# Performance work log

Hardware: AMD Instinct MI355X
Metric: run time of the kernel (lower is better)

Reference implementation:

```python
import jax, jax.numpy as jnp
import numpy as np
import math

# AF2 IPA dims
B, N = 1, 768
C1, C2 = 384, 128          # single / pair channels
H = 12                     # heads
SQK, SV = 16, 16           # scalar qk / v per head
PQK, PV = 4, 8             # point qk / v per head


def quat_to_rot(quat):
    # quat [..., 4] -> rotation matrix [..., 3, 3] (normalized, as QuatAffine.from_tensor)
    q = quat / jnp.linalg.norm(quat, axis=-1, keepdims=True)
    w, x, y, z = q[..., 0], q[..., 1], q[..., 2], q[..., 3]
    r0 = jnp.stack([1 - 2 * (y * y + z * z), 2 * (x * y - w * z), 2 * (x * z + w * y)], axis=-1)
    r1 = jnp.stack([2 * (x * y + w * z), 1 - 2 * (x * x + z * z), 2 * (y * z - w * x)], axis=-1)
    r2 = jnp.stack([2 * (x * z - w * y), 2 * (y * z + w * x), 1 - 2 * (x * x + y * y)], axis=-1)
    return jnp.stack([r0, r1, r2], axis=-2)


def setup_inputs():
    key = jax.random.key(0)
    ks = jax.random.split(key, 10)

    def lin(k, fan_in, fan_out):
        lim = 1.0 / np.sqrt(fan_in)
        kw, kb = jax.random.split(k)
        W = jax.random.uniform(kw, (fan_in, fan_out), minval=-lim, maxval=lim, dtype=jnp.float32)
        b = jax.random.uniform(kb, (fan_out,), minval=-lim, maxval=lim, dtype=jnp.float32)
        return W, b

    q_w, q_b = lin(ks[0], C1, SQK * H)
    kv_w, kv_b = lin(ks[1], C1, (SQK + SV) * H)
    qp_w, qp_b = lin(ks[2], C1, PQK * H * 3)
    kvp_w, kvp_b = lin(ks[3], C1, (PQK + PV) * H * 3)
    w2d_w, w2d_b = lin(ks[4], C2, H)
    fin_w, fin_b = lin(ks[5], H * (C2 + SV + 4 * PV), C1)

    rec_1d = jax.random.normal(ks[6], (B, N, C1), dtype=jnp.float32)
    rep_2d = jax.random.normal(ks[7], (B, N, N, C2), dtype=jnp.float32)
    rec_T = jax.random.normal(ks[8], (B, N, 7), dtype=jnp.float32)
    trainable_w = jnp.zeros((H,), dtype=jnp.float32)

    return dict(rec_1d=rec_1d, rep_2d=rep_2d, rec_T=rec_T,
                q_w=q_w, q_b=q_b, kv_w=kv_w, kv_b=kv_b,
                qp_w=qp_w, qp_b=qp_b, kvp_w=kvp_w, kvp_b=kvp_b,
                w2d_w=w2d_w, w2d_b=w2d_b, fin_w=fin_w, fin_b=fin_b,
                trainable_w=trainable_w)


def ipa_forward(rec_1d, rep_2d, rec_T, q_w, q_b, kv_w, kv_b, qp_w, qp_b,
                kvp_w, kvp_b, w2d_w, w2d_b, fin_w, fin_b, trainable_w):
    R = quat_to_rot(rec_T[..., :4])          # [B,N,3,3]
    t = rec_T[..., 4:]                       # [B,N,3]

    # scalar q/k/v: [B,N,H,S]
    q_scalar = (rec_1d @ q_w + q_b).reshape(B, N, H, SQK)
    kv_scalar = (rec_1d @ kv_w + kv_b).reshape(B, N, H, SQK + SV)
    k_scalar, v_scalar = kv_scalar[..., :SQK], kv_scalar[..., SQK:]

    # point q: split last dim into thirds (x,y,z blocks), rotate to global frame
    qp = (rec_1d @ qp_w + qp_b).reshape(B, N, 3, H * PQK)
    qp_glob = jnp.einsum('bnic,bncd->bnid', R, qp) + t[..., None]
    q_pt = jnp.transpose(qp_glob.reshape(B, N, 3, H, PQK), (0, 3, 1, 4, 2))  # [B,H,N,PQK,3]

    kvp = (rec_1d @ kvp_w + kvp_b).reshape(B, N, 3, H * (PQK + PV))
    kvp_glob = jnp.einsum('bnic,bncd->bnid', R, kvp) + t[..., None]
    kvp_pt = jnp.transpose(kvp_glob.reshape(B, N, 3, H, PQK + PV), (0, 3, 1, 4, 2))  # [B,H,N,P,3]
    k_pt, v_pt = kvp_pt[..., :PQK, :], kvp_pt[..., PQK:, :]

    # logit weights
    num_logit_terms = 3
    scalar_weights = math.sqrt(1.0 / (num_logit_terms * SQK))
    point_weights = math.sqrt(1.0 / (num_logit_terms * PQK * 9.0 / 2))
    pw = point_weights * jax.nn.softplus(trainable_w)  # [H]

    # point-distance logits: [B,H,Nq,Nk]
    dist = jnp.sum(jnp.square(q_pt[:, :, :, None, :, :] - k_pt[:, :, None, :, :, :]), axis=-1)
    attn_qk_point = -0.5 * jnp.einsum('h,bhqkp->bhqk', pw, dist)

    # scalar logits
    attn_qk_scalar = jnp.einsum('bqhs,bkhs->bhqk', scalar_weights * q_scalar, k_scalar)

    # pair bias
    attn_2d = (rep_2d @ w2d_w + w2d_b)                       # [B,N,N,H]
    attn_2d = math.sqrt(1.0 / num_logit_terms) * jnp.transpose(attn_2d, (0, 3, 1, 2))

    attn = jax.nn.softmax(attn_qk_scalar + attn_qk_point + attn_2d, axis=-1)  # [B,H,Nq,Nk]

    # scalar output
    result_scalar = jnp.einsum('bhqk,bkhs->bqhs', attn, v_scalar).reshape(B, N, H * SV)

    # point output -> back to local frame
    res_pt = jnp.einsum('bhqk,bhkpc->bhqpc', attn, v_pt)                 # [B,H,N,PV,3]
    g = jnp.transpose(res_pt, (0, 2, 4, 1, 3)).reshape(B, N, 3, H * PV)  # [B,N,3,H*PV]
    local = jnp.einsum('bnci,bncd->bnid', R, g - t[..., None])           # R^T (g - t)
    pt_norm = jnp.sqrt(1e-8 + jnp.sum(jnp.square(local), axis=2))        # [B,N,H*PV]

    # pair output
    att2d = jnp.einsum('bhij,bijc->bihc', attn, rep_2d).reshape(B, N, H * C2)

    final_act = jnp.concatenate(
        [result_scalar, local[:, :, 0], local[:, :, 1], local[:, :, 2], pt_norm, att2d], axis=-1)
    return final_act @ fin_w + fin_b  # [B,N,C1]


def reference(rec_1d, rep_2d, rec_T, q_w, q_b, kv_w, kv_b, qp_w, qp_b,
              kvp_w, kvp_b, w2d_w, w2d_b, fin_w, fin_b, trainable_w):
    return ipa_forward(rec_1d, rep_2d, rec_T, q_w, q_b, kv_w, kv_b, qp_w, qp_b,
                       kvp_w, kvp_b, w2d_w, w2d_b, fin_w, fin_b, trainable_w)
```

## Files before the change

kernel.cpp:

```cpp
#include <hip/hip_runtime.h>
#include <math.h>


namespace {
constexpr int NRES = 768;
constexpr int C1V  = 384;

constexpr size_t OFF_R     = 0;
constexpr size_t OFF_T     = 10240;
constexpr size_t OFF_PW    = 13824;
constexpr size_t OFF_W2DT  = 13952;
constexpr size_t OFF_WPACK = 16384;
constexpr size_t OFF_BPACK = 458752;
constexpr size_t OFF_PROJ  = 460800;
constexpr size_t OFF_QPT   = 1345536;
constexpr size_t OFF_KPT   = 1456128;
constexpr size_t OFF_VPTT  = 1566720;
constexpr size_t OFF_VST   = 1787904;
constexpr size_t OFF_FA    = 1935360;
constexpr size_t OFF_PART  = 3557376;
}

__global__ void k0_prep(const float* __restrict__ recT,
                        const float* __restrict__ tw,
                        const float* __restrict__ w2d,
                        float* __restrict__ ws) {
  int gid = blockIdx.x * 256 + threadIdx.x;
  if (gid < NRES) {
    float w = recT[gid*7+0], x = recT[gid*7+1], y = recT[gid*7+2], z = recT[gid*7+3];
    float inv = rsqrtf(w*w + x*x + y*y + z*z);
    w *= inv; x *= inv; y *= inv; z *= inv;
    float* r = ws + OFF_R + (size_t)gid*12;
    r[0] = 1.f-2.f*(y*y+z*z); r[1] = 2.f*(x*y-w*z);     r[2] = 2.f*(x*z+w*y);
    r[3] = 2.f*(x*y+w*z);     r[4] = 1.f-2.f*(x*x+z*z); r[5] = 2.f*(y*z-w*x);
    r[6] = 2.f*(x*z-w*y);     r[7] = 2.f*(y*z+w*x);     r[8] = 1.f-2.f*(x*x+y*y);
    float* tv = ws + OFF_T + (size_t)gid*4;
    tv[0] = recT[gid*7+4]; tv[1] = recT[gid*7+5]; tv[2] = recT[gid*7+6]; tv[3] = 0.f;
  } else if (gid < NRES + 12) {
    int h = gid - NRES;
    (ws + OFF_PW)[h] = sqrtf(1.f/54.f) * log1pf(expf(tw[h]));
  } else if (gid < NRES + 12 + 1536) {
    int idx = gid - NRES - 12;
    int h = idx % 12, c = idx / 12;
    (ws + OFF_W2DT)[h*128 + c] = w2d[c*12 + h];
  }
}

__global__ void k0b_pack(const float* __restrict__ qw,  const float* __restrict__ qb,
                         const float* __restrict__ kvw, const float* __restrict__ kvb,
                         const float* __restrict__ qpw, const float* __restrict__ qpb,
                         const float* __restrict__ kvpw,const float* __restrict__ kvpb,
                         float* __restrict__ ws) {
  int idx = blockIdx.x * 256 + threadIdx.x;
  if (idx < 384*1152) {
    int k = idx / 1152, col = idx % 1152;
    float v;
    if (col < 192)      v = qw[(size_t)k*192 + col];
    else if (col < 576) v = kvw[(size_t)k*384 + (col-192)];
    else if (col < 720) v = qpw[(size_t)k*144 + (col-576)];
    else                v = kvpw[(size_t)k*432 + (col-720)];
    (ws + OFF_WPACK)[idx] = v;
  } else if (idx < 384*1152 + 1152) {
    int col = idx - 384*1152;
    float v;
    if (col < 192)      v = qb[col];
    else if (col < 576) v = kvb[col-192];
    else if (col < 720) v = qpb[col-576];
    else                v = kvpb[col-720];
    (ws + OFF_BPACK)[col] = v;
  }
}

__global__ __launch_bounds__(256) void k1_proj(const float* __restrict__ x,
                                               float* __restrict__ ws) {
  int bi = blockIdx.x, bo = blockIdx.y, t = threadIdx.x;
  __shared__ float AsT[16*68];
  __shared__ float Bs[16*68];
  const float* W = ws + OFF_WPACK;
  float accv[4][4] = {};
  int i0 = bi*64, o0 = bo*64;
  int ti = t >> 4, to = t & 15;
  for (int kt = 0; kt < 24; kt++) {
    int k0 = kt*16;
    {
      int r = t >> 2, kq = t & 3;
      float4 a = *(const float4*)(x + (size_t)(i0+r)*C1V + k0 + kq*4);
      AsT[(kq*4+0)*68 + r] = a.x;
      AsT[(kq*4+1)*68 + r] = a.y;
      AsT[(kq*4+2)*68 + r] = a.z;
      AsT[(kq*4+3)*68 + r] = a.w;
      int kr = t >> 4, ol = t & 15;
      *(float4*)&Bs[kr*68 + ol*4] =
          *(const float4*)(W + (size_t)(k0+kr)*1152 + o0 + ol*4);
    }
    __syncthreads();
    for (int k = 0; k < 16; k++) {
      float4 a4 = *(float4*)&AsT[k*68 + ti*4];
      float4 b4 = *(float4*)&Bs[k*68 + to*4];
      accv[0][0] += a4.x*b4.x; accv[0][1] += a4.x*b4.y; accv[0][2] += a4.x*b4.z; accv[0][3] += a4.x*b4.w;
      accv[1][0] += a4.y*b4.x; accv[1][1] += a4.y*b4.y; accv[1][2] += a4.y*b4.z; accv[1][3] += a4.y*b4.w;
      accv[2][0] += a4.z*b4.x; accv[2][1] += a4.z*b4.y; accv[2][2] += a4.z*b4.z; accv[2][3] += a4.z*b4.w;
      accv[3][0] += a4.w*b4.x; accv[3][1] += a4.w*b4.y; accv[3][2] += a4.w*b4.z; accv[3][3] += a4.w*b4.w;
    }
    __syncthreads();
  }
  float* proj = ws + OFF_PROJ;
  const float* bp = ws + OFF_BPACK;
  #pragma unroll
  for (int ii = 0; ii < 4; ii++) {
    int orow = i0 + ti*4 + ii;
    int ocol = o0 + to*4;
    float4 bv = *(const float4*)(bp + ocol);
    float4 v = make_float4(accv[ii][0]+bv.x, accv[ii][1]+bv.y,
                           accv[ii][2]+bv.z, accv[ii][3]+bv.w);
    *(float4*)&proj[(size_t)orow*1152 + ocol] = v;
  }
}

__global__ __launch_bounds__(256) void k2_frames(float* __restrict__ ws) {
  int i = blockIdx.x, t = threadIdx.x;
  const float* R  = ws + OFF_R + (size_t)i*12;
  const float* tv = ws + OFF_T + (size_t)i*4;
  const float* prow = ws + OFF_PROJ + (size_t)i*1152;
  if (t < 144) {
    int d = t % 48, ci = t / 48;
    const float* qp = prow + 576;
    float v = R[ci*3+0]*qp[0*48+d] + R[ci*3+1]*qp[1*48+d] + R[ci*3+2]*qp[2*48+d] + tv[ci];
    int h = d / 4, p = d % 4;
    (ws + OFF_QPT)[(size_t)i*144 + h*12 + p*3 + ci] = v;
  }
  for (int r = 0; r < 2; r++) {
    int item = t + r*256;
    if (item < 432) {
      int d = item % 144, ci = item / 144;
      const float* kp = prow + 720;
      float v = R[ci*3+0]*kp[0*144+d] + R[ci*3+1]*kp[1*144+d] + R[ci*3+2]*kp[2*144+d] + tv[ci];
      int h = d / 12, pp = d % 12;
      if (pp < 4)
        (ws + OFF_KPT)[(size_t)i*144 + h*12 + pp*3 + ci] = v;
      else
        (ws + OFF_VPTT)[((size_t)(h*8 + (pp-4))*3 + ci)*768 + i] = v;
    }
  }
  if (t < 192) {
    int h = t / 16, s = t % 16;
    (ws + OFF_VST)[(size_t)t*768 + i] = prow[192 + h*32 + 16 + s];
  }
}

__global__ __launch_bounds__(256) void k_att(const float* __restrict__ rep,
                                             const float* __restrict__ w2db_,
                                             float* __restrict__ ws) {
  __shared__ float tile[64*132];
  __shared__ float ptile[12*64];
  __shared__ float wds[12*128];
  __shared__ float qsl[192], qptl[144];
  __shared__ float mrow[12], srow[12], frow[12], tmaxs[12], w2dbl[12], pwl[12];

  int i = blockIdx.x, t = threadIdx.x;
  int w = __builtin_amdgcn_readfirstlane(t >> 6);
  int lane = t & 63;

  for (int u = t; u < 1536; u += 256) wds[u] = (ws + OFF_W2DT)[u];
  if (t < 192) qsl[t]  = (ws + OFF_PROJ)[(size_t)i*1152 + t];
  if (t < 144) qptl[t] = (ws + OFF_QPT)[(size_t)i*144 + t];
  if (t < 12) {
    mrow[t] = -1e30f; srow[t] = 0.f;
    pwl[t] = (ws + OFF_PW)[t];
    w2dbl[t] = w2db_[t];
  }
  float acc2d[12][2];
  #pragma unroll
  for (int h = 0; h < 12; h++) { acc2d[h][0] = 0.f; acc2d[h][1] = 0.f; }
  int h0, h1 = -1;
  const float* vrow0; const float* vrow1 = nullptr;
  if (t < 192) { h0 = t >> 4; vrow0 = ws + OFF_VST + (size_t)t*768; }
  else { int u = t - 192; h0 = u/24; vrow0 = ws + OFF_VPTT + (size_t)u*768; }
  if (t < 224) { int u = t + 64; h1 = u/24; vrow1 = ws + OFF_VPTT + (size_t)u*768; }
  float accV0 = 0.f, accV1 = 0.f;
  __syncthreads();

  const float sw  = 0.14433756729740643f;
  const float c2d = 0.5773502691896258f;

  for (int tt = 0; tt < 12; tt++) {
    int j0 = tt*64;
    #pragma unroll
    for (int k = 0; k < 8; k++) {
      int u = t + k*256;
      int row = u >> 5, c4 = u & 31;
      *(float4*)&tile[row*132 + c4*4] =
          *(const float4*)&rep[((size_t)i*768 + (j0+row))*128 + c4*4];
    }
    __syncthreads();

    float a2d[3] = {0.f, 0.f, 0.f};
    for (int c4 = 0; c4 < 32; c4++) {
      float4 v = *(float4*)&tile[lane*132 + c4*4];
      #pragma unroll
      for (int hh = 0; hh < 3; hh++) {
        float4 wv = *(float4*)&wds[(w*3+hh)*128 + c4*4];
        a2d[hh] += v.x*wv.x + v.y*wv.y + v.z*wv.z + v.w*wv.w;
      }
    }
    int j = j0 + lane;
    const float* ksr  = ws + OFF_PROJ + (size_t)j*1152 + 192;
    const float* kptr = ws + OFF_KPT + (size_t)j*144;
    float l[3], tm[3];
    #pragma unroll
    for (int hh = 0; hh < 3; hh++) {
      int h = w*3 + hh;
      float ds_ = 0.f;
      #pragma unroll
      for (int s4 = 0; s4 < 4; s4++) {
        float4 q4 = *(const float4*)(qsl + h*16 + s4*4);
        float4 k4 = *(const float4*)(ksr + h*32 + s4*4);
        ds_ += q4.x*k4.x + q4.y*k4.y + q4.z*k4.z + q4.w*k4.w;
      }
      float dp = 0.f;
      #pragma unroll
      for (int pc = 0; pc < 3; pc++) {
        float4 q4 = *(const float4*)(qptl + h*12 + pc*4);
        float4 k4 = *(const float4*)(kptr + h*12 + pc*4);
        float dx = q4.x-k4.x, dy = q4.y-k4.y, dz = q4.z-k4.z, dw = q4.w-k4.w;
        dp += dx*dx + dy*dy + dz*dz + dw*dw;
      }
      l[hh] = sw*ds_ - 0.5f*pwl[h]*dp + c2d*(a2d[hh] + w2dbl[h]);
      float m = l[hh];
      #pragma unroll
      for (int d = 1; d < 64; d <<= 1) m = fmaxf(m, __shfl_xor(m, d));
      tm[hh] = m;
    }
    if (lane == 0) {
      tmaxs[w*3+0] = tm[0]; tmaxs[w*3+1] = tm[1]; tmaxs[w*3+2] = tm[2];
    }
    __syncthreads();

    if (t < 12) {
      float mo = mrow[t];
      float mn = fmaxf(mo, tmaxs[t]);
      frow[t] = __expf(mo - mn);
      mrow[t] = mn;
    }
    __syncthreads();

    #pragma unroll
    for (int hh = 0; hh < 3; hh++) {
      int h = w*3 + hh;
      float p = __expf(l[hh] - mrow[h]);
      ptile[h*64 + lane] = p;
      float s = p;
      #pragma unroll
      for (int d = 1; d < 64; d <<= 1) s += __shfl_xor(s, d);
      if (lane == 0) srow[h] = srow[h]*frow[h] + s;
    }
    __syncthreads();

    #pragma unroll
    for (int h = 0; h < 12; h++) {
      float fh = frow[h];
      acc2d[h][0] *= fh; acc2d[h][1] *= fh;
    }
    int jb = w*16;
    for (int jj = 0; jj < 16; jj++) {
      int jl = jb + jj;
      float2 r2 = *(float2*)&tile[jl*132 + lane*2];
      #pragma unroll
      for (int h = 0; h < 12; h++) {
        float p = ptile[h*64 + jl];
        acc2d[h][0] += p*r2.x; acc2d[h][1] += p*r2.y;
      }
    }
    {
      float a = accV0 * frow[h0];
      const float* vr = vrow0 + j0;
      for (int q = 0; q < 16; q++) {
        float4 v4 = *(const float4*)(vr + q*4);
        a += ptile[h0*64+q*4+0]*v4.x + ptile[h0*64+q*4+1]*v4.y
           + ptile[h0*64+q*4+2]*v4.z + ptile[h0*64+q*4+3]*v4.w;
      }
      accV0 = a;
    }
    if (h1 >= 0) {
      float a = accV1 * frow[h1];
      const float* vr = vrow1 + j0;
      for (int q = 0; q < 16; q++) {
        float4 v4 = *(const float4*)(vr + q*4);
        a += ptile[h1*64+q*4+0]*v4.x + ptile[h1*64+q*4+1]*v4.y
           + ptile[h1*64+q*4+2]*v4.z + ptile[h1*64+q*4+3]*v4.w;
      }
      accV1 = a;
    }
    __syncthreads();
  }

  float* fa = ws + OFF_FA + (size_t)i*2112;
  float* respt = ptile;
  if (t < 192) fa[t] = accV0 / srow[h0];
  else respt[t - 192] = accV0 / srow[h0];
  if (h1 >= 0) respt[t + 64] = accV1 / srow[h1];
  float* redbuf = tile;
  #pragma unroll
  for (int h = 0; h < 12; h++) {
    redbuf[w*1536 + h*128 + lane*2 + 0] = acc2d[h][0];
    redbuf[w*1536 + h*128 + lane*2 + 1] = acc2d[h][1];
  }
  __syncthreads();
  for (int r = 0; r < 6; r++) {
    int u = t + r*256;
    int h = u >> 7;
    float v = redbuf[u] + redbuf[1536+u] + redbuf[3072+u] + redbuf[4608+u];
    fa[576 + u] = v / srow[h];
  }
  if (t < 96) {
    const float* R  = ws + OFF_R + (size_t)i*12;
    const float* tv = ws + OFF_T + (size_t)i*4;
    float g0 = respt[t*3+0] - tv[0];
    float g1 = respt[t*3+1] - tv[1];
    float g2 = respt[t*3+2] - tv[2];
    float l0 = R[0]*g0 + R[3]*g1 + R[6]*g2;
    float l1 = R[1]*g0 + R[4]*g1 + R[7]*g2;
    float l2 = R[2]*g0 + R[5]*g1 + R[8]*g2;
    fa[192 + 0*96 + t] = l0;
    fa[192 + 1*96 + t] = l1;
    fa[192 + 2*96 + t] = l2;
    fa[480 + t] = sqrtf(1e-8f + l0*l0 + l1*l1 + l2*l2);
  }
}

__global__ __launch_bounds__(256) void k7_gemm(const float* __restrict__ finw,
                                               float* __restrict__ ws) {
  int bi = blockIdx.x, bo = blockIdx.y, bz = blockIdx.z, t = threadIdx.x;
  __shared__ float AsT[16*68];
  __shared__ float Bs[16*68];
  const float* fa = ws + OFF_FA;
  float accv[4][4] = {};
  int i0 = bi*64, o0 = bo*64;
  int ti = t >> 4, to = t & 15;
  for (int kt = 0; kt < 33; kt++) {
    int k0 = bz*528 + kt*16;
    {
      int r = t >> 2, kq = t & 3;
      float4 a = *(const float4*)(fa + (size_t)(i0+r)*2112 + k0 + kq*4);
      AsT[(kq*4+0)*68 + r] = a.x;
      AsT[(kq*4+1)*68 + r] = a.y;
      AsT[(kq*4+2)*68 + r] = a.z;
      AsT[(kq*4+3)*68 + r] = a.w;
      int kr = t >> 4, ol = t & 15;
      *(float4*)&Bs[kr*68 + ol*4] =
          *(const float4*)(finw + (size_t)(k0+kr)*384 + o0 + ol*4);
    }
    __syncthreads();
    for (int k = 0; k < 16; k++) {
      float4 a4 = *(float4*)&AsT[k*68 + ti*4];
      float4 b4 = *(float4*)&Bs[k*68 + to*4];
      accv[0][0] += a4.x*b4.x; accv[0][1] += a4.x*b4.y; accv[0][2] += a4.x*b4.z; accv[0][3] += a4.x*b4.w;
      accv[1][0] += a4.y*b4.x; accv[1][1] += a4.y*b4.y; accv[1][2] += a4.y*b4.z; accv[1][3] += a4.y*b4.w;
      accv[2][0] += a4.z*b4.x; accv[2][1] += a4.z*b4.y; accv[2][2] += a4.z*b4.z; accv[2][3] += a4.z*b4.w;
      accv[3][0] += a4.w*b4.x; accv[3][1] += a4.w*b4.y; accv[3][2] += a4.w*b4.z; accv[3][3] += a4.w*b4.w;
    }
    __syncthreads();
  }
  float* part = ws + OFF_PART + (size_t)bz*768*384;
  #pragma unroll
  for (int ii = 0; ii < 4; ii++) {
    float4 v = make_float4(accv[ii][0], accv[ii][1], accv[ii][2], accv[ii][3]);
    *(float4*)&part[(size_t)(i0 + ti*4 + ii)*384 + o0 + to*4] = v;
  }
}

__global__ void k8_out(const float* __restrict__ finb,
                       const float* __restrict__ ws,
                       float* __restrict__ out) {
  int idx = blockIdx.x*256 + threadIdx.x;
  int o = idx % 384;
  const float* part = ws + OFF_PART;
  out[idx] = part[idx] + part[294912 + idx] + part[2*294912 + idx]
           + part[3*294912 + idx] + finb[o];
}

extern "C" void kernel_launch(void* const* d_in, const int* in_sizes, int n_in,
                              void* d_out, int out_size, void* d_ws, size_t ws_size,
                              hipStream_t stream) {
  const float* rec1d = (const float*)d_in[0];
  const float* rep2d = (const float*)d_in[1];
  const float* recT  = (const float*)d_in[2];
  const float* qw    = (const float*)d_in[3];
  const float* qb    = (const float*)d_in[4];
  const float* kvw   = (const float*)d_in[5];
  const float* kvb   = (const float*)d_in[6];
  const float* qpw   = (const float*)d_in[7];
  const float* qpb   = (const float*)d_in[8];
  const float* kvpw  = (const float*)d_in[9];
  const float* kvpb  = (const float*)d_in[10];
  const float* w2dw  = (const float*)d_in[11];
  const float* w2db  = (const float*)d_in[12];
  const float* finw  = (const float*)d_in[13];
  const float* finb  = (const float*)d_in[14];
  const float* tw    = (const float*)d_in[15];
  float* ws  = (float*)d_ws;
  float* out = (float*)d_out;

  hipLaunchKernelGGL(k0_prep, dim3(10), dim3(256), 0, stream, recT, tw, w2dw, ws);
  hipLaunchKernelGGL(k0b_pack, dim3(1733), dim3(256), 0, stream,
                     qw, qb, kvw, kvb, qpw, qpb, kvpw, kvpb, ws);
  hipLaunchKernelGGL(k1_proj, dim3(12, 18), dim3(256), 0, stream, rec1d, ws);
  hipLaunchKernelGGL(k2_frames, dim3(768), dim3(256), 0, stream, ws);
  hipLaunchKernelGGL(k_att, dim3(768), dim3(256), 0, stream, rep2d, w2db, ws);
  hipLaunchKernelGGL(k7_gemm, dim3(12, 6, 4), dim3(256), 0, stream, finw, ws);
  hipLaunchKernelGGL(k8_out, dim3(1152), dim3(256), 0, stream, finb, ws, out);
}
```

Baseline: 0.9998 ms.

## Split attention over key chunks with wave-local softmax and a combine kernel

Measured after the change: 2.980 ms. +198.1%, slower.

```diff
diff --git a/kernel.cpp b/kernel.cpp
--- a/kernel.cpp
+++ b/kernel.cpp
@@ -18,6 +18,7 @@
 constexpr size_t OFF_VPTT  = 1566720;
 constexpr size_t OFF_VST   = 1787904;
 constexpr size_t OFF_FA    = 1935360;
+constexpr size_t OFF_PARTIAL = 3557376;
 constexpr size_t OFF_PART  = 3557376;
 }
 
@@ -148,43 +149,52 @@
   }
 }
 
-__global__ __launch_bounds__(256) void k_att(const float* __restrict__ rep,
-                                             const float* __restrict__ w2db_,
-                                             float* __restrict__ ws) {
+__global__ __launch_bounds__(256, 3) void k_att2(const float* __restrict__ rep,
+                                                 const float* __restrict__ w2db_,
+                                                 float* __restrict__ ws) {
   __shared__ float tile[64*132];
-  __shared__ float ptile[12*64];
+  __shared__ float ptile[12*68];
   __shared__ float wds[12*128];
   __shared__ float qsl[192], qptl[144];
-  __shared__ float mrow[12], srow[12], frow[12], tmaxs[12], w2dbl[12], pwl[12];
-
-  int i = blockIdx.x, t = threadIdx.x;
-  int w = __builtin_amdgcn_readfirstlane(t >> 6);
-  int lane = t & 63;
+
+  int jc = blockIdx.x, i = blockIdx.y, t = threadIdx.x;
+  int w = t >> 6, lane = t & 63;
+  int hb = w*3;
 
   for (int u = t; u < 1536; u += 256) wds[u] = (ws + OFF_W2DT)[u];
   if (t < 192) qsl[t]  = (ws + OFF_PROJ)[(size_t)i*1152 + t];
   if (t < 144) qptl[t] = (ws + OFF_QPT)[(size_t)i*144 + t];
-  if (t < 12) {
-    mrow[t] = -1e30f; srow[t] = 0.f;
-    pwl[t] = (ws + OFF_PW)[t];
-    w2dbl[t] = w2db_[t];
-  }
-  float acc2d[12][2];
+  float pwv[3], w2dbv[3];
   #pragma unroll
-  for (int h = 0; h < 12; h++) { acc2d[h][0] = 0.f; acc2d[h][1] = 0.f; }
-  int h0, h1 = -1;
-  const float* vrow0; const float* vrow1 = nullptr;
-  if (t < 192) { h0 = t >> 4; vrow0 = ws + OFF_VST + (size_t)t*768; }
-  else { int u = t - 192; h0 = u/24; vrow0 = ws + OFF_VPTT + (size_t)u*768; }
-  if (t < 224) { int u = t + 64; h1 = u/24; vrow1 = ws + OFF_VPTT + (size_t)u*768; }
+  for (int hh = 0; hh < 3; hh++) {
+    pwv[hh]   = (ws + OFF_PW)[hb+hh];
+    w2dbv[hh] = w2db_[hb+hh];
+  }
+  float m0 = -1e30f, m1 = -1e30f, m2 = -1e30f;
+  float s0 = 0.f, s1 = 0.f, s2 = 0.f;
+  float a2d0[2] = {0.f,0.f}, a2d1[2] = {0.f,0.f}, a2d2[2] = {0.f,0.f};
+
+  int hh0 = (lane < 40) ? 0 : 1;
+  int idx0 = lane - hh0*40;
+  const float* vrow0 = (idx0 < 16)
+      ? ws + OFF_VST  + (size_t)((hb+hh0)*16 + idx0)*768
+      : ws + OFF_VPTT + (size_t)((hb+hh0)*24 + idx0-16)*768;
+  int pr0 = (hb+hh0)*68;
+  int s1i = lane + 64;
+  bool has1 = s1i < 120;
+  int hh1 = (s1i < 80) ? 1 : 2;
+  int idx1 = s1i - hh1*40;
+  const float* vrow1 = (idx1 < 16)
+      ? ws + OFF_VST  + (size_t)((hb+hh1)*16 + idx1)*768
+      : ws + OFF_VPTT + (size_t)((hb+hh1)*24 + idx1-16)*768;
+  int pr1 = (hb+hh1)*68;
   float accV0 = 0.f, accV1 = 0.f;
-  __syncthreads();
 
   const float sw  = 0.14433756729740643f;
   const float c2d = 0.5773502691896258f;
 
-  for (int tt = 0; tt < 12; tt++) {
-    int j0 = tt*64;
+  for (int tt = 0; tt < 3; tt++) {
+    int j0 = jc*192 + tt*64;
     #pragma unroll
     for (int k = 0; k < 8; k++) {
       int u = t + k*256;
@@ -199,17 +209,17 @@
       float4 v = *(float4*)&tile[lane*132 + c4*4];
       #pragma unroll
       for (int hh = 0; hh < 3; hh++) {
-        float4 wv = *(float4*)&wds[(w*3+hh)*128 + c4*4];
+        float4 wv = *(float4*)&wds[(hb+hh)*128 + c4*4];
         a2d[hh] += v.x*wv.x + v.y*wv.y + v.z*wv.z + v.w*wv.w;
       }
     }
     int j = j0 + lane;
     const float* ksr  = ws + OFF_PROJ + (size_t)j*1152 + 192;
     const float* kptr = ws + OFF_KPT + (size_t)j*144;
-    float l[3], tm[3];
+    float l[3];
     #pragma unroll
     for (int hh = 0; hh < 3; hh++) {
-      int h = w*3 + hh;
+      int h = hb + hh;
       float ds_ = 0.f;
       #pragma unroll
       for (int s4 = 0; s4 < 4; s4++) {
@@ -225,93 +235,147 @@
         float dx = q4.x-k4.x, dy = q4.y-k4.y, dz = q4.z-k4.z, dw = q4.w-k4.w;
         dp += dx*dx + dy*dy + dz*dz + dw*dw;
       }
-      l[hh] = sw*ds_ - 0.5f*pwl[h]*dp + c2d*(a2d[hh] + w2dbl[h]);
-      float m = l[hh];
-      #pragma unroll
-      for (int d = 1; d < 64; d <<= 1) m = fmaxf(m, __shfl_xor(m, d));
-      tm[hh] = m;
-    }
-    if (lane == 0) {
-      tmaxs[w*3+0] = tm[0]; tmaxs[w*3+1] = tm[1]; tmaxs[w*3+2] = tm[2];
-    }
-    __syncthreads();
-
-    if (t < 12) {
-      float mo = mrow[t];
-      float mn = fmaxf(mo, tmaxs[t]);
-      frow[t] = __expf(mo - mn);
-      mrow[t] = mn;
-    }
-    __syncthreads();
-
-    #pragma unroll
-    for (int hh = 0; hh < 3; hh++) {
-      int h = w*3 + hh;
-      float p = __expf(l[hh] - mrow[h]);
-      ptile[h*64 + lane] = p;
-      float s = p;
-      #pragma unroll
-      for (int d = 1; d < 64; d <<= 1) s += __shfl_xor(s, d);
-      if (lane == 0) srow[h] = srow[h]*frow[h] + s;
-    }
-    __syncthreads();
-
-    #pragma unroll
-    for (int h = 0; h < 12; h++) {
-      float fh = frow[h];
-      acc2d[h][0] *= fh; acc2d[h][1] *= fh;
-    }
-    int jb = w*16;
-    for (int jj = 0; jj < 16; jj++) {
-      int jl = jb + jj;
-      float2 r2 = *(float2*)&tile[jl*132 + lane*2];
-      #pragma unroll
-      for (int h = 0; h < 12; h++) {
-        float p = ptile[h*64 + jl];
-        acc2d[h][0] += p*r2.x; acc2d[h][1] += p*r2.y;
-      }
-    }
-    {
-      float a = accV0 * frow[h0];
+      l[hh] = sw*ds_ - 0.5f*pwv[hh]*dp + c2d*(a2d[hh] + w2dbv[hh]);
+    }
+
+    float f0, f1, f2;
+    {
+      float mt = l[0];
+      #pragma unroll
+      for (int d = 1; d < 64; d <<= 1) mt = fmaxf(mt, __shfl_xor(mt, d));
+      float mn = fmaxf(m0, mt); f0 = __expf(m0 - mn); m0 = mn;
+      float p = __expf(l[0] - mn); ptile[(hb+0)*68 + lane] = p;
+      float ss = p;
+      #pragma unroll
+      for (int d = 1; d < 64; d <<= 1) ss += __shfl_xor(ss, d);
+      s0 = s0*f0 + ss;
+    }
+    {
+      float mt = l[1];
+      #pragma unroll
+      for (int d = 1; d < 64; d <<= 1) mt = fmaxf(mt, __shfl_xor(mt, d));
+      float mn = fmaxf(m1, mt); f1 = __expf(m1 - mn); m1 = mn;
+      float p = __expf(l[1] - mn); ptile[(hb+1)*68 + lane] = p;
+      float ss = p;
+      #pragma unroll
+      for (int d = 1; d < 64; d <<= 1) ss += __shfl_xor(ss, d);
+      s1 = s1*f1 + ss;
+    }
+    {
+      float mt = l[2];
+      #pragma unroll
+      for (int d = 1; d < 64; d <<= 1) mt = fmaxf(mt, __shfl_xor(mt, d));
+      float mn = fmaxf(m2, mt); f2 = __expf(m2 - mn); m2 = mn;
+      float p = __expf(l[2] - mn); ptile[(hb+2)*68 + lane] = p;
+      float ss = p;
+      #pragma unroll
+      for (int d = 1; d < 64; d <<= 1) ss += __shfl_xor(ss, d);
+      s2 = s2*f2 + ss;
+    }
+
+    a2d0[0] *= f0; a2d0[1] *= f0;
+    a2d1[0] *= f1; a2d1[1] *= f1;
+    a2d2[0] *= f2; a2d2[1] *= f2;
+    for (int jq = 0; jq < 16; jq++) {
+      float4 p0 = *(float4*)&ptile[(hb+0)*68 + jq*4];
+      float4 p1 = *(float4*)&ptile[(hb+1)*68 + jq*4];
+      float4 p2 = *(float4*)&ptile[(hb+2)*68 + jq*4];
+      #pragma unroll
+      for (int r = 0; r < 4; r++) {
+        float2 r2 = *(float2*)&tile[(jq*4+r)*132 + lane*2];
+        float pa = (r==0)?p0.x:(r==1)?p0.y:(r==2)?p0.z:p0.w;
+        float pb = (r==0)?p1.x:(r==1)?p1.y:(r==2)?p1.z:p1.w;
+        float pc = (r==0)?p2.x:(r==1)?p2.y:(r==2)?p2.z:p2.w;
+        a2d0[0] += pa*r2.x; a2d0[1] += pa*r2.y;
+        a2d1[0] += pb*r2.x; a2d1[1] += pb*r2.y;
+        a2d2[0] += pc*r2.x; a2d2[1] += pc*r2.y;
+      }
+    }
+
+    {
+      float fsel = (lane < 40) ? f0 : f1;
+      float a = accV0 * fsel;
       const float* vr = vrow0 + j0;
       for (int q = 0; q < 16; q++) {
         float4 v4 = *(const float4*)(vr + q*4);
-        a += ptile[h0*64+q*4+0]*v4.x + ptile[h0*64+q*4+1]*v4.y
-           + ptile[h0*64+q*4+2]*v4.z + ptile[h0*64+q*4+3]*v4.w;
+        float4 p4 = *(float4*)&ptile[pr0 + q*4];
+        a += p4.x*v4.x + p4.y*v4.y + p4.z*v4.z + p4.w*v4.w;
       }
       accV0 = a;
     }
-    if (h1 >= 0) {
-      float a = accV1 * frow[h1];
+    if (has1) {
+      float fsel = (s1i < 80) ? f1 : f2;
+      float a = accV1 * fsel;
       const float* vr = vrow1 + j0;
       for (int q = 0; q < 16; q++) {
         float4 v4 = *(const float4*)(vr + q*4);
-        a += ptile[h1*64+q*4+0]*v4.x + ptile[h1*64+q*4+1]*v4.y
-           + ptile[h1*64+q*4+2]*v4.z + ptile[h1*64+q*4+3]*v4.w;
+        float4 p4 = *(float4*)&ptile[pr1 + q*4];
+        a += p4.x*v4.x + p4.y*v4.y + p4.z*v4.z + p4.w*v4.w;
       }
       accV1 = a;
     }
     __syncthreads();
   }
 
+  float* part = ws + OFF_PARTIAL + ((size_t)i*4 + jc)*2048;
+  if (lane == 0) {
+    part[hb+0] = m0; part[hb+1] = m1; part[hb+2] = m2;
+    part[12+hb+0] = s0; part[12+hb+1] = s1; part[12+hb+2] = s2;
+  }
+  part[24 + (hb+0)*128 + lane*2 + 0] = a2d0[0];
+  part[24 + (hb+0)*128 + lane*2 + 1] = a2d0[1];
+  part[24 + (hb+1)*128 + lane*2 + 0] = a2d1[0];
+  part[24 + (hb+1)*128 + lane*2 + 1] = a2d1[1];
+  part[24 + (hb+2)*128 + lane*2 + 0] = a2d2[0];
+  part[24 + (hb+2)*128 + lane*2 + 1] = a2d2[1];
+  {
+    int dst0 = (idx0 < 16) ? 1560 + (hb+hh0)*16 + idx0
+                           : 1752 + (hb+hh0)*24 + (idx0-16);
+    part[dst0] = accV0;
+  }
+  if (has1) {
+    int dst1 = (idx1 < 16) ? 1560 + (hb+hh1)*16 + idx1
+                           : 1752 + (hb+hh1)*24 + (idx1-16);
+    part[dst1] = accV1;
+  }
+}
+
+__global__ __launch_bounds__(256) void k_comb(float* __restrict__ ws) {
+  int i = blockIdx.x, t = threadIdx.x;
+  __shared__ float coef[4][12];
+  __shared__ float respt[288];
+  const float* P = ws + OFF_PARTIAL + (size_t)i*4*2048;
+  if (t < 12) {
+    float ma = P[t], mb = P[2048+t], mc = P[4096+t], md = P[6144+t];
+    float M = fmaxf(fmaxf(ma,mb), fmaxf(mc,md));
+    float ea = __expf(ma-M), eb = __expf(mb-M), ec = __expf(mc-M), ed = __expf(md-M);
+    float S = P[12+t]*ea + P[2048+12+t]*eb + P[4096+12+t]*ec + P[6144+12+t]*ed;
+    float inv = 1.f/S;
+    coef[0][t] = ea*inv; coef[1][t] = eb*inv; coef[2][t] = ec*inv; coef[3][t] = ed*inv;
+  }
+  __syncthreads();
   float* fa = ws + OFF_FA + (size_t)i*2112;
-  float* respt = ptile;
-  if (t < 192) fa[t] = accV0 / srow[h0];
-  else respt[t - 192] = accV0 / srow[h0];
-  if (h1 >= 0) respt[t + 64] = accV1 / srow[h1];
-  float* redbuf = tile;
-  #pragma unroll
-  for (int h = 0; h < 12; h++) {
-    redbuf[w*1536 + h*128 + lane*2 + 0] = acc2d[h][0];
-    redbuf[w*1536 + h*128 + lane*2 + 1] = acc2d[h][1];
-  }
-  __syncthreads();
   for (int r = 0; r < 6; r++) {
     int u = t + r*256;
     int h = u >> 7;
-    float v = redbuf[u] + redbuf[1536+u] + redbuf[3072+u] + redbuf[4608+u];
-    fa[576 + u] = v / srow[h];
-  }
+    fa[576+u] = P[24+u]*coef[0][h] + P[2048+24+u]*coef[1][h]
+              + P[4096+24+u]*coef[2][h] + P[6144+24+u]*coef[3][h];
+  }
+  if (t < 192) {
+    int h = t >> 4;
+    fa[t] = P[1560+t]*coef[0][h] + P[2048+1560+t]*coef[1][h]
+          + P[4096+1560+t]*coef[2][h] + P[6144+1560+t]*coef[3][h];
+  }
+  #pragma unroll
+  for (int r = 0; r < 2; r++) {
+    int u = t + r*256;
+    if (u < 288) {
+      int h = u / 24;
+      respt[u] = P[1752+u]*coef[0][h] + P[2048+1752+u]*coef[1][h]
+               + P[4096+1752+u]*coef[2][h] + P[6144+1752+u]*coef[3][h];
+    }
+  }
+  __syncthreads();
   if (t < 96) {
     const float* R  = ws + OFF_R + (size_t)i*12;
     const float* tv = ws + OFF_T + (size_t)i*4;
@@ -406,7 +470,8 @@
                      qw, qb, kvw, kvb, qpw, qpb, kvpw, kvpb, ws);
   hipLaunchKernelGGL(k1_proj, dim3(12, 18), dim3(256), 0, stream, rec1d, ws);
   hipLaunchKernelGGL(k2_frames, dim3(768), dim3(256), 0, stream, ws);
-  hipLaunchKernelGGL(k_att, dim3(768), dim3(256), 0, stream, rep2d, w2db, ws);
+  hipLaunchKernelGGL(k_att2, dim3(4, 768), dim3(256), 0, stream, rep2d, w2db, ws);
+  hipLaunchKernelGGL(k_comb, dim3(768), dim3(256), 0, stream, ws);
   hipLaunchKernelGGL(k7_gemm, dim3(12, 6, 4), dim3(256), 0, stream, finw, ws);
   hipLaunchKernelGGL(k8_out, dim3(1152), dim3(256), 0, stream, finb, ws, out);
 }
```
